# Kernel tuning notes

Measured on AMD Instinct MI355X. Metric: run time of the kernel, lower is better.

Reference implementation:

```python
import jax, jax.numpy as jnp
import numpy as np

EPS = 1e-8
SMOOTH = 9.0
N_IMAGE, N_REGIONS, N_CAP, MAX_WORDS = 64, 36, 64, 40
EMBED, SIM_DIM = 1024, 256


def l2norm(x, axis=-1):
    n = jnp.sqrt(jnp.sum(x * x, axis=axis, keepdims=True)) + EPS
    return x / n


def setup_inputs() -> dict:
    key = jax.random.key(0)
    k1, k2, k3, k4 = jax.random.split(key, 4)
    img_emb = jax.random.normal(k1, (N_IMAGE, N_REGIONS, EMBED), dtype=jnp.float32)
    cap_emb = jax.random.normal(k2, (N_CAP, MAX_WORDS, EMBED), dtype=jnp.float32)
    cap_lens = jax.random.randint(k3, (N_CAP,), 10, MAX_WORDS + 1)
    # zero out padded words so the batched formulation matches the per-caption loop
    mask = (jnp.arange(MAX_WORDS)[None, :] < cap_lens[:, None]).astype(jnp.float32)
    cap_emb = cap_emb * mask[:, :, None]
    adjs = jnp.zeros((N_CAP, MAX_WORDS, MAX_WORDS), dtype=jnp.int32)
    depends = jnp.zeros((N_CAP, MAX_WORDS, MAX_WORDS), dtype=jnp.int32)
    r = np.sqrt(6.0) / np.sqrt(EMBED + SIM_DIM)
    W = jax.random.uniform(k4, (EMBED, SIM_DIM), minval=-r, maxval=r, dtype=jnp.float32)
    b = jnp.zeros((SIM_DIM,), dtype=jnp.float32)
    return {"img_emb": img_emb, "cap_emb": cap_emb, "cap_lens": cap_lens,
            "adjs": adjs, "depends": depends, "W": W, "b": b}


def reference(img_emb, cap_emb, cap_lens, adjs, depends, W, b):
    C, L, D = cap_emb.shape
    mask = (jnp.arange(L)[None, :] < cap_lens[:, None]).astype(cap_emb.dtype)  # (C, L)
    cap = cap_emb * mask[:, :, None]
    # attn: (C, I, R, L) = context . query^T for every (caption, image) pair
    attn = jnp.einsum('ird,cld->cirl', img_emb, cap)
    attn = jax.nn.leaky_relu(attn, negative_slope=0.1)
    # l2norm over the word dim (padded words contribute exactly 0)
    attn = attn / (jnp.sqrt(jnp.sum(attn * attn, axis=3, keepdims=True)) + EPS)
    # softmax over regions after transpose + smooth scaling: (C, I, L, R)
    attn = jax.nn.softmax(jnp.swapaxes(attn, 2, 3) * SMOOTH, axis=3)
    wc = jnp.einsum('cilr,ird->cild', attn, img_emb)  # (C, I, L, D)
    wc = l2norm(wc, axis=-1)
    sim = jnp.square(wc - cap[:, None, :, :])
    out = l2norm(jax.nn.relu(sim @ W + b), axis=-1)
    # zero padded-word rows (the original returns only :n_word slices)
    out = out * mask[:, None, :, None]
    return out  # (C, I, L, SIM_DIM)
```

## Files before the change

kernel.cpp:

```cpp
#include <hip/hip_runtime.h>

#define C_N 64
#define I_N 64
#define R_N 36
#define L_N 40
#define D_N 1024
#define S_N 256

#define P_LD 72

#define OFF_CAP 2359296
#define OFF_WT  4980736
#define OFF_IMT 5242880
#define OFF_SLK 8388608
#define OFF_SIM 8388672
#define M_ALL   (C_N * I_N * L_N)
#define CH_STRIDE ((size_t)M_ALL * 32)
#define OFF_G   (OFF_SIM + 32 * CH_STRIDE)

typedef float f4 __attribute__((ext_vector_type(4)));
typedef short s16x8 __attribute__((ext_vector_type(8)));
typedef short s16x4 __attribute__((ext_vector_type(4)));

__device__ __forceinline__ unsigned short f2bs(float f) {
    union { float f; unsigned u; } v; v.f = f;
    unsigned r = v.u + 0x7FFFu + ((v.u >> 16) & 1u);
    return (unsigned short)(r >> 16);
}
__device__ __forceinline__ float bs2f(unsigned short s) {
    union { unsigned u; float f; } v; v.u = ((unsigned)s) << 16;
    return v.f;
}
__device__ __forceinline__ void async16(const unsigned short* g, unsigned short* l) {
    __builtin_amdgcn_global_load_lds(
        (const __attribute__((address_space(1))) unsigned int*)g,
        (__attribute__((address_space(3))) unsigned int*)l, 16, 0, 0);
}

__global__ void k_convert(const float* __restrict__ img, const float* __restrict__ cap,
                          const float* __restrict__ W, unsigned short* __restrict__ ws) {
    int t = blockIdx.x * 256 + threadIdx.x;
    if (t < I_N * R_N * D_N) ws[t] = f2bs(img[t]);
    if (t < C_N * L_N * D_N) ws[OFF_CAP + t] = f2bs(cap[t]);
    if (t < D_N * S_N) {
        int d = t >> 8, s = t & 255;
        ws[OFF_WT + (((d >> 5) * 256 + s) * 32) + (d & 31)] = f2bs(W[t]);
    }
    if (t < 64) ws[OFF_SLK + t] = 0;
}

__global__ __launch_bounds__(256)
void k_imt(const float* __restrict__ img, unsigned short* __restrict__ imt) {
    __shared__ unsigned short t[64][50];
    const int i = blockIdx.y, d0 = blockIdx.x * 64;
    const int tid = threadIdx.x;
    #pragma unroll
    for (int it = 0; it < 9; ++it) {
        int e = it * 256 + tid;
        int r = e >> 6, dc = e & 63;
        t[dc][r] = f2bs(img[((size_t)i * R_N + r) * D_N + d0 + dc]);
    }
    #pragma unroll
    for (int it = 0; it < 3; ++it) {
        int e = it * 256 + tid;
        t[e & 63][36 + (e >> 6)] = 0;
    }
    __syncthreads();
    #pragma unroll
    for (int it = 0; it < 6; ++it) {
        int e = it * 256 + tid;
        int dc = e / 24, wd = e - dc * 24;
        unsigned v = (unsigned)t[dc][2 * wd] | ((unsigned)t[dc][2 * wd + 1] << 16);
        ((unsigned*)imt)[(size_t)(i * D_N + d0 + dc) * 24 + wd] = v;
    }
}

__global__ __launch_bounds__(64)
void k_gram(const unsigned short* __restrict__ img_b, unsigned short* __restrict__ g) {
    const int i = blockIdx.x;
    const int lane = threadIdx.x;
    const int q = lane >> 4, ln16 = lane & 15;
    const unsigned short* ai = img_b + i * (R_N * D_N);
    unsigned short* gi = g + i * (48 * 64);
    for (int e = lane; e < 48 * 8; e += 64) {
        int r = e >> 3, wd = e & 7;
        ((unsigned*)(gi + r * 64 + 48))[wd] = 0;
    }
    f4 c[3][3] = {};
    #pragma unroll 4
    for (int ks = 0; ks < 32; ++ks) {
        const int kb = ks * 32 + q * 8;
        s16x8 af[3];
        af[0] = *(const s16x8*)(ai + ln16 * D_N + kb);
        af[1] = *(const s16x8*)(ai + (16 + ln16) * D_N + kb);
        af[2] = (ln16 < 4) ? *(const s16x8*)(ai + (32 + ln16) * D_N + kb) : (s16x8)0;
        #pragma unroll
        for (int mt = 0; mt < 3; ++mt)
            #pragma unroll
            for (int nt = 0; nt < 3; ++nt)
                c[mt][nt] = __builtin_amdgcn_mfma_f32_16x16x32_bf16(af[mt], af[nt], c[mt][nt], 0, 0, 0);
    }
    #pragma unroll
    for (int mt = 0; mt < 3; ++mt)
        #pragma unroll
        for (int nt = 0; nt < 3; ++nt)
            #pragma unroll
            for (int j = 0; j < 4; ++j)
                gi[(mt * 16 + q * 4 + j) * 64 + nt * 16 + ln16] = f2bs(c[mt][nt][j]);
}

__global__ __launch_bounds__(512, 4)
void k_pre(const unsigned short* __restrict__ img_b,
           const unsigned short* __restrict__ cap_b,
           const unsigned short* __restrict__ img_t,
           const unsigned short* __restrict__ gram,
           unsigned short* __restrict__ simg) {
    __shared__ __align__(16) unsigned short s_p[8][48 * P_LD];

    const int n = blockIdx.y * 8 + blockIdx.x;
    const int x = n & 7, m = n >> 3;
    const int i   = ((x & 3) << 4) | (m >> 2);
    const int oct = ((x >> 2) << 2) | (m & 3);
    const int wave = threadIdx.x >> 6, lane = threadIdx.x & 63;
    const int c = oct * 8 + wave;
    const int pair = c * I_N + i;
    const int q = lane >> 4, ln16 = lane & 15;

    const unsigned short* ai = img_b + i * (R_N * D_N);
    const unsigned short* bc = cap_b + c * (L_N * D_N);
    const unsigned short* imtc = img_t + (size_t)i * D_N * 48;
    unsigned short* sp = &s_p[wave][0];

    for (int k = lane; k < 48 * P_LD / 2; k += 64) ((unsigned*)sp)[k] = 0;

    f4 acc[3][3] = {};
    #pragma unroll 4
    for (int ks = 0; ks < 32; ++ks) {
        const int kb = ks * 32 + q * 8;
        s16x8 af[3], bf[3];
        af[0] = *(const s16x8*)(ai + ln16 * D_N + kb);
        af[1] = *(const s16x8*)(ai + (16 + ln16) * D_N + kb);
        af[2] = (ln16 < 4) ? *(const s16x8*)(ai + (32 + ln16) * D_N + kb) : (s16x8)0;
        bf[0] = *(const s16x8*)(bc + ln16 * D_N + kb);
        bf[1] = *(const s16x8*)(bc + (16 + ln16) * D_N + kb);
        bf[2] = (ln16 < 8) ? *(const s16x8*)(bc + (32 + ln16) * D_N + kb) : (s16x8)0;
        #pragma unroll
        for (int mt = 0; mt < 3; ++mt)
            #pragma unroll
            for (int nt = 0; nt < 3; ++nt)
                acc[mt][nt] = __builtin_amdgcn_mfma_f32_16x16x32_bf16(af[mt], bf[nt], acc[mt][nt], 0, 0, 0);
    }

    #pragma unroll
    for (int mt = 0; mt < 3; ++mt)
        #pragma unroll
        for (int nt = 0; nt < 3; ++nt)
            #pragma unroll
            for (int j = 0; j < 4; ++j) {
                float v = acc[mt][nt][j];
                acc[mt][nt][j] = (v > 0.f) ? v : 0.1f * v;
            }
    #pragma unroll
    for (int mt = 0; mt < 3; ++mt)
        #pragma unroll
        for (int j = 0; j < 4; ++j) {
            float ss = 0.f;
            #pragma unroll
            for (int nt = 0; nt < 3; ++nt) ss += acc[mt][nt][j] * acc[mt][nt][j];
            #pragma unroll
            for (int o = 1; o < 16; o <<= 1) ss += __shfl_xor(ss, o, 64);
            float inv = 1.f / (sqrtf(ss) + 1e-8f);
            #pragma unroll
            for (int nt = 0; nt < 3; ++nt) acc[mt][nt][j] *= inv;
        }
    #pragma unroll
    for (int nt = 0; nt < 3; ++nt) {
        const int l = nt * 16 + ln16;
        float mx = -1e30f;
        #pragma unroll
        for (int mt = 0; mt < 3; ++mt)
            #pragma unroll
            for (int j = 0; j < 4; ++j) {
                int r = mt * 16 + q * 4 + j;
                if (r < R_N) mx = fmaxf(mx, 9.f * acc[mt][nt][j]);
            }
        mx = fmaxf(mx, __shfl_xor(mx, 16, 64));
        mx = fmaxf(mx, __shfl_xor(mx, 32, 64));
        float sum = 0.f;
        #pragma unroll
        for (int mt = 0; mt < 3; ++mt)
            #pragma unroll
            for (int j = 0; j < 4; ++j) {
                int r = mt * 16 + q * 4 + j;
                float e = (r < R_N) ? __expf(9.f * acc[mt][nt][j] - mx) : 0.f;
                acc[mt][nt][j] = e;
                sum += e;
            }
        sum += __shfl_xor(sum, 16, 64);
        sum += __shfl_xor(sum, 32, 64);
        float inv = 1.f / sum;
        #pragma unroll
        for (int mt = 0; mt < 3; ++mt)
            #pragma unroll
            for (int j = 0; j < 4; ++j) {
                int r = mt * 16 + q * 4 + j;
                if (r < R_N && l < L_N) sp[l * P_LD + r] = f2bs(acc[mt][nt][j] * inv);
            }
    }

    s16x8 paf[3][2];
    #pragma unroll
    for (int nl = 0; nl < 3; ++nl)
        #pragma unroll
        for (int ks = 0; ks < 2; ++ks)
            paf[nl][ks] = *(const s16x8*)(sp + (nl * 16 + ln16) * P_LD + ks * 32 + q * 8);

    const unsigned short* gi = gram + i * (48 * 64);
    f4 T[3][3] = {};
    #pragma unroll
    for (int ks = 0; ks < 2; ++ks) {
        const int kb = ks * 32 + q * 8;
        s16x8 ga[3];
        #pragma unroll
        for (int mt = 0; mt < 3; ++mt)
            ga[mt] = *(const s16x8*)(gi + (mt * 16 + ln16) * 64 + kb);
        #pragma unroll
        for (int mt = 0; mt < 3; ++mt)
            #pragma unroll
            for (int nl = 0; nl < 3; ++nl)
                T[mt][nl] = __builtin_amdgcn_mfma_f32_16x16x32_bf16(ga[mt], paf[nl][ks], T[mt][nl], 0, 0, 0);
    }
    float inv2[3];
    #pragma unroll
    for (int nl = 0; nl < 3; ++nl) {
        const int l = nl * 16 + ln16;
        float rsl = 0.f;
        #pragma unroll
        for (int mt = 0; mt < 3; ++mt) {
            const s16x4 pv = *(const s16x4*)(sp + l * P_LD + mt * 16 + q * 4);
            #pragma unroll
            for (int j = 0; j < 4; ++j)
                rsl += bs2f((unsigned short)pv[j]) * T[mt][nl][j];
        }
        rsl += __shfl_xor(rsl, 16, 64);
        rsl += __shfl_xor(rsl, 32, 64);
        inv2[nl] = 1.f / (sqrtf(rsl) + 1e-8f);
    }

    #pragma unroll 2
    for (int ch = 0; ch < 32; ++ch) {
        f4 a2[2][3] = {};
        #pragma unroll
        for (int ks = 0; ks < 2; ++ks) {
            const int kb = ks * 32 + q * 8;
            #pragma unroll
            for (int md = 0; md < 2; ++md) {
                const int drow = ch * 32 + md * 16 + ln16;
                s16x8 afr = *(const s16x8*)(imtc + drow * 48 + kb);
                #pragma unroll
                for (int nl = 0; nl < 3; ++nl)
                    a2[md][nl] = __builtin_amdgcn_mfma_f32_16x16x32_bf16(afr, paf[nl][ks], a2[md][nl], 0, 0, 0);
            }
        }
        const size_t chbase = (size_t)ch * CH_STRIDE + (size_t)pair * L_N * 32;
        #pragma unroll
        for (int nl = 0; nl < 3; ++nl) {
            const int l = nl * 16 + ln16;
            if (l < L_N) {
                const float iv = inv2[nl];
                #pragma unroll
                for (int md = 0; md < 2; ++md) {
                    const int dd = md * 16 + q * 4;
                    const int db = ch * 32 + dd;
                    const s16x4 cv = *(const s16x4*)(bc + l * D_N + db);
                    s16x4 ov;
                    #pragma unroll
                    for (int j = 0; j < 4; ++j) {
                        float dv = a2[md][nl][j] * iv - bs2f((unsigned short)cv[j]);
                        ov[j] = (short)f2bs(dv * dv);
                    }
                    __builtin_nontemporal_store(ov,
                        (s16x4*)(simg + chbase + (size_t)l * 32 + dd));
                }
            }
        }
    }
}

__global__ __launch_bounds__(512, 4)
void k_gemm3(const unsigned short* __restrict__ simt,
             const unsigned short* __restrict__ wtt,
             const int* __restrict__ cap_lens,
             const float* __restrict__ bias,
             float* __restrict__ out) {
    __shared__ __align__(16) unsigned short sA[2][128 * 32];
    __shared__ __align__(16) unsigned short sB[2][256 * 32];
    __shared__ float s_sum[128];

    const int tid = threadIdx.x;
    const int w = tid >> 6, lane = tid & 63;
    const int ln16 = lane & 15, q = lane >> 4;
    const int wm = (w >> 2) * 64, wn = (w & 3) * 64;
    const int m0 = blockIdx.x * 128;
    const int srow = tid >> 2;
    const int swz = ((tid & 3) ^ ((srow >> 1) & 3)) << 3;
    const unsigned short* gA  = simt + ((size_t)(m0 + srow)) * 32 + swz;
    const unsigned short* gB0 = wtt + (size_t)srow * 32 + swz;
    const unsigned short* gB1 = wtt + (size_t)(128 + srow) * 32 + swz;
    unsigned short* const lA = (unsigned short*)sA + tid * 8;
    unsigned short* const lB = (unsigned short*)sB + tid * 8;

    if (tid < 128) s_sum[tid] = 0.f;

    async16(gA, lA);
    async16(gB0, lB);
    async16(gB1, lB + 4096);

    f4 acc[4][4] = {};
    #pragma unroll 1
    for (int kc = 0; kc < 31; ++kc) {
        const int nb = (kc + 1) & 1;
        async16(gA + (size_t)(kc + 1) * CH_STRIDE, lA + nb * 4096);
        async16(gB0 + (kc + 1) * 8192, lB + nb * 8192);
        async16(gB1 + (kc + 1) * 8192, lB + nb * 8192 + 4096);
        asm volatile("s_waitcnt vmcnt(3)" ::: "memory");
        __builtin_amdgcn_s_barrier();
        __builtin_amdgcn_sched_barrier(0);
        const unsigned short* cA = (const unsigned short*)sA + (kc & 1) * 4096;
        const unsigned short* cB = (const unsigned short*)sB + (kc & 1) * 8192;
        s16x8 af[4], bf[4];
        #pragma unroll
        for (int mt = 0; mt < 4; ++mt) {
            int row = wm + mt * 16 + ln16;
            af[mt] = *(const s16x8*)(cA + row * 32 + ((q ^ ((row >> 1) & 3)) << 3));
        }
        #pragma unroll
        for (int nt = 0; nt < 4; ++nt) {
            int row = wn + nt * 16 + ln16;
            bf[nt] = *(const s16x8*)(cB + row * 32 + ((q ^ ((row >> 1) & 3)) << 3));
        }
        #pragma unroll
        for (int mt = 0; mt < 4; ++mt)
            #pragma unroll
            for (int nt = 0; nt < 4; ++nt)
                acc[mt][nt] = __builtin_amdgcn_mfma_f32_16x16x32_bf16(af[mt], bf[nt], acc[mt][nt], 0, 0, 0);
        __builtin_amdgcn_s_barrier();
    }
    asm volatile("s_waitcnt vmcnt(0)" ::: "memory");
    __builtin_amdgcn_s_barrier();
    __builtin_amdgcn_sched_barrier(0);
    {
        const unsigned short* cA = (const unsigned short*)sA + 4096;
        const unsigned short* cB = (const unsigned short*)sB + 8192;
        s16x8 af[4], bf[4];
        #pragma unroll
        for (int mt = 0; mt < 4; ++mt) {
            int row = wm + mt * 16 + ln16;
            af[mt] = *(const s16x8*)(cA + row * 32 + ((q ^ ((row >> 1) & 3)) << 3));
        }
        #pragma unroll
        for (int nt = 0; nt < 4; ++nt) {
            int row = wn + nt * 16 + ln16;
            bf[nt] = *(const s16x8*)(cB + row * 32 + ((q ^ ((row >> 1) & 3)) << 3));
        }
        #pragma unroll
        for (int mt = 0; mt < 4; ++mt)
            #pragma unroll
            for (int nt = 0; nt < 4; ++nt)
                acc[mt][nt] = __builtin_amdgcn_mfma_f32_16x16x32_bf16(af[mt], bf[nt], acc[mt][nt], 0, 0, 0);
    }

    float bv[4];
    #pragma unroll
    for (int nt = 0; nt < 4; ++nt) bv[nt] = bias[wn + nt * 16 + ln16];
    #pragma unroll
    for (int mt = 0; mt < 4; ++mt)
        #pragma unroll
        for (int j = 0; j < 4; ++j) {
            float s = 0.f;
            #pragma unroll
            for (int nt = 0; nt < 4; ++nt) {
                float v = acc[mt][nt][j] + bv[nt];
                v = fmaxf(v, 0.f);
                acc[mt][nt][j] = v;
                s += v * v;
            }
            #pragma unroll
            for (int o = 1; o < 16; o <<= 1) s += __shfl_xor(s, o, 64);
            if (ln16 == 0) atomicAdd(&s_sum[wm + mt * 16 + q * 4 + j], s);
        }
    __syncthreads();
    if (tid < 128) {
        int grow = m0 + tid;
        int c = grow / (I_N * L_N);
        int l = grow % L_N;
        float inv = 1.f / (sqrtf(s_sum[tid]) + 1e-8f);
        s_sum[tid] = (l < cap_lens[c]) ? inv : 0.f;
    }
    __syncthreads();
    #pragma unroll
    for (int mt = 0; mt < 4; ++mt)
        #pragma unroll
        for (int j = 0; j < 4; ++j) {
            const int rt = wm + mt * 16 + q * 4 + j;
            const float sc = s_sum[rt];
            #pragma unroll
            for (int nt = 0; nt < 4; ++nt)
                __builtin_nontemporal_store(acc[mt][nt][j] * sc,
                    &out[(size_t)(m0 + rt) * S_N + wn + nt * 16 + ln16]);
        }
}

extern "C" void kernel_launch(void* const* d_in, const int* in_sizes, int n_in,
                              void* d_out, int out_size, void* d_ws, size_t ws_size,
                              hipStream_t stream) {
    const float* img  = (const float*)d_in[0];
    const float* cap  = (const float*)d_in[1];
    const int*   lens = (const int*)d_in[2];
    const float* W    = (const float*)d_in[5];
    const float* bias = (const float*)d_in[6];
    float* out = (float*)d_out;
    unsigned short* ws = (unsigned short*)d_ws;

    k_convert<<<10240, 256, 0, stream>>>(img, cap, W, ws);
    dim3 gridT(16, I_N);
    k_imt<<<gridT, 256, 0, stream>>>(img, ws + OFF_IMT);
    k_gram<<<I_N, 64, 0, stream>>>(ws, ws + OFF_G);

    dim3 gridP(8, I_N);
    k_pre<<<gridP, 512, 0, stream>>>(ws, ws + OFF_CAP, ws + OFF_IMT, ws + OFF_G,
                                     ws + OFF_SIM);

    k_gemm3<<<M_ALL / 128, 512, 0, stream>>>(ws + OFF_SIM, ws + OFF_WT, lens, bias, out);
}
```

Baseline: 521.5 us.

## Permute K layout for 16-byte sim stores and reverse gemm3 chunk order

The W transposed layout is permuted within each 32-wide K chunk so that the producer kernel can pack both md halves into a single 16-byte nontemporal store instead of two 8-byte stores. Because the permutation is applied consistently to A and B in K, the dot product is unchanged. The final GEMM also walks the K chunks in reverse order, so it begins with the most recently written channel, which is more likely still cached in L2/MALL. This relies on the sim and W layouts staying in sync.

```diff
diff --git a/kernel.cpp b/kernel.cpp
--- a/kernel.cpp
+++ b/kernel.cpp
@@ -18,6 +18,7 @@
 #define CH_STRIDE ((size_t)M_ALL * 32)
 #define OFF_G   (OFF_SIM + 32 * CH_STRIDE)
 
+
 typedef float f4 __attribute__((ext_vector_type(4)));
 typedef short s16x8 __attribute__((ext_vector_type(8)));
 typedef short s16x4 __attribute__((ext_vector_type(4)));
@@ -44,7 +45,10 @@
     if (t < C_N * L_N * D_N) ws[OFF_CAP + t] = f2bs(cap[t]);
     if (t < D_N * S_N) {
         int d = t >> 8, s = t & 255;
-        ws[OFF_WT + (((d >> 5) * 256 + s) * 32) + (d & 31)] = f2bs(W[t]);
+        int ch = d >> 5, wi = d & 31;
+        int md = wi >> 4, r = wi & 15, q = r >> 2, j = r & 3;
+        int ep = q * 8 + md * 4 + j;
+        ws[OFF_WT + ((ch * 256 + s) * 32) + ep] = f2bs(W[t]);
     }
     if (t < 64) ws[OFF_SLK + t] = 0;
 }
@@ -268,20 +272,19 @@
             const int l = nl * 16 + ln16;
             if (l < L_N) {
                 const float iv = inv2[nl];
+                s16x8 ov;
                 #pragma unroll
                 for (int md = 0; md < 2; ++md) {
-                    const int dd = md * 16 + q * 4;
-                    const int db = ch * 32 + dd;
+                    const int db = ch * 32 + md * 16 + q * 4;
                     const s16x4 cv = *(const s16x4*)(bc + l * D_N + db);
-                    s16x4 ov;
                     #pragma unroll
                     for (int j = 0; j < 4; ++j) {
                         float dv = a2[md][nl][j] * iv - bs2f((unsigned short)cv[j]);
-                        ov[j] = (short)f2bs(dv * dv);
+                        ov[md * 4 + j] = (short)f2bs(dv * dv);
                     }
-                    __builtin_nontemporal_store(ov,
-                        (s16x4*)(simg + chbase + (size_t)l * 32 + dd));
                 }
+                __builtin_nontemporal_store(ov,
+                    (s16x8*)(simg + chbase + (size_t)l * 32 + q * 8));
             }
         }
     }
@@ -312,22 +315,23 @@
 
     if (tid < 128) s_sum[tid] = 0.f;
 
-    async16(gA, lA);
-    async16(gB0, lB);
-    async16(gB1, lB + 4096);
+    async16(gA + (size_t)31 * CH_STRIDE, lA);
+    async16(gB0 + 31 * 8192, lB);
+    async16(gB1 + 31 * 8192, lB + 4096);
 
     f4 acc[4][4] = {};
     #pragma unroll 1
-    for (int kc = 0; kc < 31; ++kc) {
-        const int nb = (kc + 1) & 1;
-        async16(gA + (size_t)(kc + 1) * CH_STRIDE, lA + nb * 4096);
-        async16(gB0 + (kc + 1) * 8192, lB + nb * 8192);
-        async16(gB1 + (kc + 1) * 8192, lB + nb * 8192 + 4096);
+    for (int t = 0; t < 31; ++t) {
+        const int nb = (t + 1) & 1;
+        const int pch = 30 - t;
+        async16(gA + (size_t)pch * CH_STRIDE, lA + nb * 4096);
+        async16(gB0 + pch * 8192, lB + nb * 8192);
+        async16(gB1 + pch * 8192, lB + nb * 8192 + 4096);
         asm volatile("s_waitcnt vmcnt(3)" ::: "memory");
         __builtin_amdgcn_s_barrier();
         __builtin_amdgcn_sched_barrier(0);
-        const unsigned short* cA = (const unsigned short*)sA + (kc & 1) * 4096;
-        const unsigned short* cB = (const unsigned short*)sB + (kc & 1) * 8192;
+        const unsigned short* cA = (const unsigned short*)sA + (t & 1) * 4096;
+        const unsigned short* cB = (const unsigned short*)sB + (t & 1) * 8192;
         s16x8 af[4], bf[4];
         #pragma unroll
         for (int mt = 0; mt < 4; ++mt) {
```

Measured after the change: 508.7 us. -2.5%, faster.
